# Performance work log

Measured on AMD Instinct MI355X. Metric: run time of the kernel, lower is better.

The kernel has to match this reference:

```python
import jax, jax.numpy as jnp
import numpy as np

VOCAB, VDIM, DDIM, BATCH = 50257, 300, 512, 16


def setup_inputs() -> dict:
    key = jax.random.key(0)
    k1, k2, k3, k4, k5 = jax.random.split(key, 5)
    return {
        "decoder_hidden": jax.random.normal(k1, (BATCH, DDIM), dtype=jnp.float32),
        "embedding_vocab": jax.random.normal(k2, (VOCAB, VDIM), dtype=jnp.float32),
        "W_dec": jax.random.normal(k3, (VDIM, DDIM), dtype=jnp.float32) * (1.0 / np.sqrt(DDIM)),
        "b_dec": jax.random.normal(k4, (VDIM,), dtype=jnp.float32) * 0.01,
        "W_full": jax.random.normal(k5, (VDIM,), dtype=jnp.float32) * (1.0 / np.sqrt(VDIM)),
        "b_full": jnp.zeros((), dtype=jnp.float32),
    }


def reference(decoder_hidden, embedding_vocab, W_dec, b_dec, W_full, b_full):
    # query: (B, vocab_dim) = decoder_att(decoder_hidden)
    query = decoder_hidden @ W_dec.T + b_dec
    # additive scores: relu(vocab + query) projected to scalar -> (B, V)
    hidden = jax.nn.relu(embedding_vocab[None, :, :] + query[:, None, :])  # (B, V, D)
    att = jnp.einsum("bvd,d->bv", hidden, W_full) + b_full
    alpha = jax.nn.softmax(att, axis=1)  # softmax over vocab
    # weighted sum of vocab embeddings: (B, vocab_dim)
    attention_weighted_encoding = jnp.einsum("bv,vd->bd", alpha, embedding_vocab)
    return attention_weighted_encoding, alpha
```

## Files before the change

kernel.cpp:

```cpp
#include <hip/hip_runtime.h>

constexpr int V  = 50257;
constexpr int D  = 300;
constexpr int KD = 512;
constexpr int B  = 16;

constexpr int ROWS = 64;
constexpr int NB_ATT = (V + ROWS - 1) / ROWS;
constexpr int NT = 5;
constexpr int NC  = 512;
constexpr int RPC = (V + NC - 1) / NC;

constexpr float NEG_HUGE = -1.0e30f;

constexpr size_t WS_QT   = 0;
constexpr size_t WS_STAT = 4800;
constexpr size_t WS_MS   = WS_STAT + (size_t)NB_ATT * 32;
constexpr size_t WS_PART = WS_MS + 32;
constexpr size_t WS_TMP  = WS_PART + (size_t)NC * 4800;

struct f4 { float v[4]; };
__device__ __forceinline__ f4 ld4(const float* p) {
    float4 t = *(const float4*)p;
    return {t.x, t.y, t.z, t.w};
}

#define AS1 __attribute__((address_space(1)))
#define AS3 __attribute__((address_space(3)))
#define DPPF(x, CTRL) __int_as_float(__builtin_amdgcn_mov_dpp(__float_as_int(x), (CTRL), 0xF, 0xF, false))

__global__ void __launch_bounds__(256) k_query(
    const float* __restrict__ dh, const float* __restrict__ Wdec,
    const float* __restrict__ bdec, float* __restrict__ q_t)
{
    int wid  = (blockIdx.x * 256 + threadIdx.x) >> 6;
    int lane = threadIdx.x & 63;
    if (wid >= D * B) return;
    int d = wid >> 4, b = wid & 15;
    const float* wrow = Wdec + (size_t)d * KD;
    const float* hrow = dh + (size_t)b * KD;
    float s = 0.f;
    for (int k = lane; k < KD; k += 64) s += wrow[k] * hrow[k];
    #pragma unroll
    for (int off = 32; off; off >>= 1) s += __shfl_down(s, off, 64);
    if (lane == 0) q_t[d * 16 + b] = s + bdec[d];
}

__global__ void __launch_bounds__(256) k_att(
    const float* __restrict__ E, const float* __restrict__ q_t,
    const float* __restrict__ wf, const float* __restrict__ bf,
    float* __restrict__ att, float* __restrict__ blkstats)
{
    __shared__ float se[3 * 4096];
    __shared__ float sq[5120];
    __shared__ float sw[320];

    const int t    = threadIdx.x;
    const int slot = t & 15;
    const int rg   = t >> 4;
    const int s4   = slot << 2;
    const int v0   = blockIdx.x * ROWS;

    for (int i = t; i < 5120; i += 256) {
        int d = i >> 4, b = i & 15;
        int bq = b >> 2, bl = b & 3;
        float v = (d < D) ? q_t[d * 16 + b] : 0.f;
        int P = (d >> 1) * 8 + ((((d & 1) << 2) | bq) ^ ((d >> 2) & 7));
        sq[P * 4 + bl] = v;
    }
    for (int i = t; i < 320; i += 256) sw[i] = (i < D) ? wf[i] : 0.f;

    int xq[2][4];
    #pragma unroll
    for (int i1 = 0; i1 < 2; ++i1)
        #pragma unroll
        for (int bq = 0; bq < 4; ++bq)
            xq[i1][bq] = slot * 64 + 4 * ((((i1 << 2) | bq)) ^ (slot & 7));

    float acc[4][16];
    #pragma unroll
    for (int j = 0; j < 4; ++j)
        #pragma unroll
        for (int b = 0; b < 16; ++b) acc[j][b] = 0.f;

    __syncthreads();

#define STAGE(TT, BI) do {                                                    \
    int dd = (TT) * 64 + s4;                                                  \
    if (dd >= D) dd = 0;                         \
    _Pragma("unroll")                                                         \
    for (int jj = 0; jj < 4; ++jj) {                                          \
        int row = v0 + jj * 16 + rg;                                          \
        if (row >= V) row = V - 1;                                            \
        const float* src = E + (size_t)row * D + dd;                          \
        float* lb = se + (BI) * 4096 + jj * 1024 + (t << 2);                  \
        __builtin_amdgcn_global_load_lds((const AS1 void*)src,                \
                                         (AS3 void*)lb, 16, 0, 0);            \
    }                                                                         \
} while (0)

#define COMPUTE(TT, BI) do {                                                  \
    const float* buf = se + (BI) * 4096;                                      \
    f4 ej[4];                                                                 \
    _Pragma("unroll")                                                         \
    for (int j = 0; j < 4; ++j) ej[j] = ld4(buf + rg * 64 + j * 1024 + s4);   \
    f4 wv = ld4(sw + (TT) * 64 + s4);                                         \
    const float* sqt = sq + (TT) * 1024;                                      \
    _Pragma("unroll")                                                         \
    for (int i = 0; i < 4; ++i) {                                             \
        float wi = wv.v[i];                                                   \
        _Pragma("unroll")                                                     \
        for (int bq = 0; bq < 4; ++bq) {                                      \
            f4 qv = ld4(sqt + (i >> 1) * 32 + xq[i & 1][bq]);                 \
            _Pragma("unroll")                                                 \
            for (int j = 0; j < 4; ++j) {                                     \
                float e = ej[j].v[i];                                         \
                _Pragma("unroll")                                             \
                for (int bl = 0; bl < 4; ++bl)                                \
                    acc[j][bq * 4 + bl] =                                     \
                        fmaf(fmaxf(e + qv.v[bl], 0.f), wi,                    \
                             acc[j][bq * 4 + bl]);                            \
            }                                                                 \
        }                                                                     \
    }                                                                         \
} while (0)

    STAGE(0, 0);
    STAGE(1, 1);
    for (int tt = 0; tt < NT; ++tt) {
        __builtin_amdgcn_sched_barrier(0);
        if (tt < NT - 1) asm volatile("s_waitcnt vmcnt(4)" ::: "memory");
        else             asm volatile("s_waitcnt vmcnt(0)" ::: "memory");
        __builtin_amdgcn_s_barrier();
        __builtin_amdgcn_sched_barrier(0);
        if (tt + 2 < NT) STAGE(tt + 2, (tt + 2) % 3);
        COMPUTE(tt, tt % 3);
    }
#undef STAGE
#undef COMPUTE

    #pragma unroll
    for (int j = 0; j < 4; ++j)
        #pragma unroll
        for (int b = 0; b < 16; ++b) {
            float x = acc[j][b];
            x += DPPF(x, 0xB1);
            x += DPPF(x, 0x4E);
            acc[j][b] = x;
        }
    const int c = slot & 3;
    float kept[4][4];
    #pragma unroll
    for (int j = 0; j < 4; ++j)
        #pragma unroll
        for (int kk = 0; kk < 4; ++kk) {
            float x = (c == 0) ? acc[j][kk]
                    : (c == 1) ? acc[j][4 + kk]
                    : (c == 2) ? acc[j][8 + kk]
                    :            acc[j][12 + kk];
            x += __shfl_xor(x, 4, 64);
            x += __shfl_xor(x, 8, 64);
            kept[j][kk] = x;
        }

    __syncthreads();
    float* smsM = se;
    float* smsS = se + 1024;

    const float bfull = bf[0];
    const int g = (t >> 6) * 16 + (rg & 3) * 4 + (slot >> 2);
    const int jown = slot >> 2;
    const int rowown = v0 + rg + 16 * jown;
    const bool okown = rowown < V;

    #pragma unroll
    for (int kk = 0; kk < 4; ++kk) {
        const int b = 4 * c + kk;
        float x = ((jown == 0) ? kept[0][kk] : (jown == 1) ? kept[1][kk]
                 : (jown == 2) ? kept[2][kk] : kept[3][kk]) + bfull;
        if (okown) att[(size_t)b * V + rowown] = x;
        smsM[g * 16 + b] = okown ? x : NEG_HUGE;
        smsS[g * 16 + b] = okown ? 1.f : 0.f;
    }
    __syncthreads();
    if (t < 64) {
        int b = t & 15, q4 = t >> 4;
        float m = NEG_HUGE, s = 0.f;
        for (int u = 0; u < 16; ++u) {
            int gg = q4 * 16 + u;
            float mg = smsM[gg * 16 + b], sg = smsS[gg * 16 + b];
            float mn = fmaxf(m, mg);
            s = s * __expf(m - mn) + sg * __expf(mg - mn);
            m = mn;
        }
        se[2048 + q4 * 16 + b] = m;
        se[2112 + q4 * 16 + b] = s;
    }
    __syncthreads();
    if (t < 16) {
        float m = NEG_HUGE, s = 0.f;
        #pragma unroll
        for (int q4 = 0; q4 < 4; ++q4) {
            float mg = se[2048 + q4 * 16 + t], sg = se[2112 + q4 * 16 + t];
            float mn = fmaxf(m, mg);
            s = s * __expf(m - mn) + sg * __expf(mg - mn);
            m = mn;
        }
        blkstats[((size_t)blockIdx.x * 16 + t) * 2]     = m;
        blkstats[((size_t)blockIdx.x * 16 + t) * 2 + 1] = s;
    }
}

__global__ void __launch_bounds__(64) k_combine(
    const float* __restrict__ blkstats, float* __restrict__ MS)
{
    int b = blockIdx.x, lane = threadIdx.x;
    float m = NEG_HUGE;
    for (int cc = lane; cc < NB_ATT; cc += 64)
        m = fmaxf(m, blkstats[(size_t)(cc * 16 + b) * 2]);
    #pragma unroll
    for (int off = 32; off; off >>= 1) m = fmaxf(m, __shfl_xor(m, off, 64));
    float s = 0.f;
    for (int cc = lane; cc < NB_ATT; cc += 64)
        s += blkstats[(size_t)(cc * 16 + b) * 2 + 1] *
             __expf(blkstats[(size_t)(cc * 16 + b) * 2] - m);
    #pragma unroll
    for (int off = 32; off; off >>= 1) s += __shfl_xor(s, off, 64);
    if (lane == 0) { MS[b * 2] = m; MS[b * 2 + 1] = 1.f / s; }
}

__global__ void __launch_bounds__(320) k_awsum(
    const float* __restrict__ E, float* __restrict__ att,
    const float* __restrict__ MS, float* __restrict__ partials)
{
    __shared__ float sal[RPC * 16];
    int c = blockIdx.x, t = threadIdx.x;
    int v0 = c * RPC;
    int n = V - v0;
    if (n > RPC) n = RPC;
    if (n < 0) n = 0;

    for (int i = t; i < RPC * 16; i += 320) {
        int b = i / RPC, vv = i - b * RPC;
        float a = 0.f;
        if (vv < n) {
            float M = MS[b * 2], invS = MS[b * 2 + 1];
            size_t gi = (size_t)b * V + v0 + vv;
            a = __expf(att[gi] - M) * invS;
            att[gi] = a;
        }
        sal[vv * 16 + b] = a;
    }
    __syncthreads();

    if (t < D) {
        float acc[16];
        #pragma unroll
        for (int b = 0; b < 16; ++b) acc[b] = 0.f;
        #pragma unroll 4
        for (int vv = 0; vv < n; ++vv) {
            float e = E[(size_t)(v0 + vv) * D + t];
            const float* ap = sal + vv * 16;
            f4 a0 = ld4(ap), a1 = ld4(ap + 4), a2 = ld4(ap + 8), a3 = ld4(ap + 12);
            #pragma unroll
            for (int b = 0; b < 4; ++b) {
                acc[b]      = fmaf(a0.v[b], e, acc[b]);
                acc[b + 4]  = fmaf(a1.v[b], e, acc[b + 4]);
                acc[b + 8]  = fmaf(a2.v[b], e, acc[b + 8]);
                acc[b + 12] = fmaf(a3.v[b], e, acc[b + 12]);
            }
        }
        #pragma unroll
        for (int b = 0; b < 16; ++b)
            partials[(size_t)c * 4800 + b * D + t] = acc[b];
    }
}

__global__ void __launch_bounds__(256) k_red1(
    const float* __restrict__ partials, float* __restrict__ tmp)
{
    int o4 = blockIdx.x * 256 + threadIdx.x;
    if (o4 >= 1200) return;
    int y = blockIdx.y;
    float4 s = {0.f, 0.f, 0.f, 0.f};
    for (int c = y * 32; c < y * 32 + 32; ++c) {
        float4 p = *(const float4*)(partials + (size_t)c * 4800 + o4 * 4);
        s.x += p.x; s.y += p.y; s.z += p.z; s.w += p.w;
    }
    *(float4*)(tmp + (size_t)y * 4800 + o4 * 4) = s;
}

__global__ void __launch_bounds__(256) k_red2(
    const float* __restrict__ tmp, float* __restrict__ out)
{
    int o4 = blockIdx.x * 256 + threadIdx.x;
    if (o4 >= 1200) return;
    float4 s = {0.f, 0.f, 0.f, 0.f};
    #pragma unroll
    for (int y = 0; y < 16; ++y) {
        float4 p = *(const float4*)(tmp + (size_t)y * 4800 + o4 * 4);
        s.x += p.x; s.y += p.y; s.z += p.z; s.w += p.w;
    }
    *(float4*)(out + o4 * 4) = s;
}

extern "C" void kernel_launch(void* const* d_in, const int* in_sizes, int n_in,
                              void* d_out, int out_size, void* d_ws, size_t ws_size,
                              hipStream_t stream) {
    const float* dh   = (const float*)d_in[0];
    const float* E    = (const float*)d_in[1];
    const float* Wdec = (const float*)d_in[2];
    const float* bdec = (const float*)d_in[3];
    const float* wf   = (const float*)d_in[4];
    const float* bf   = (const float*)d_in[5];
    float* out = (float*)d_out;
    float* ws  = (float*)d_ws;

    float* q_t   = ws + WS_QT;
    float* stats = ws + WS_STAT;
    float* MS    = ws + WS_MS;
    float* part  = ws + WS_PART;
    float* tmp   = ws + WS_TMP;
    float* att   = out + 4800;

    k_query<<<(D * B + 3) / 4, 256, 0, stream>>>(dh, Wdec, bdec, q_t);
    k_att<<<NB_ATT, 256, 0, stream>>>(E, q_t, wf, bf, att, stats);
    k_combine<<<B, 64, 0, stream>>>(stats, MS);
    k_awsum<<<NC, 320, 0, stream>>>(E, att, MS, part);
    k_red1<<<dim3(5, 16), 256, 0, stream>>>(part, tmp);
    k_red2<<<5, 256, 0, stream>>>(tmp, out);
}
```

Before: 91.56 us.

## Restructure attention-score kernel with register-resident query, packed FMA and online softmax

The score kernel now keeps the query and W_full slices in registers as float2 vectors and uses packed max/FMA operations. It stages contiguous 16-row chunks of the embedding into double-buffered LDS instead of column-tiled triple buffers. Row sums are reduced with cross-lane shuffles, and running softmax max/sum statistics are kept per thread, which replaces the earlier two-level LDS reduction. The weighted-sum kernel switches to 448 chunks with more unrolling, with the reduction split adjusted to match. This trades the prior register-tiled outer-product reuse for fewer LDS reads of the query, at the cost of extra shuffles and more block syncs per chunk.

Result: faster. 87.66 us (-4.3%).

```diff
diff --git a/kernel.cpp b/kernel.cpp
--- a/kernel.cpp
+++ b/kernel.cpp
@@ -6,18 +6,19 @@
 constexpr int B  = 16;
 
 constexpr int ROWS = 64;
-constexpr int NB_ATT = (V + ROWS - 1) / ROWS;
-constexpr int NT = 5;
-constexpr int NC  = 512;
-constexpr int RPC = (V + NC - 1) / NC;
+constexpr int NBLK = (V + ROWS - 1) / ROWS;
+constexpr int NC  = 448;
+constexpr int RPC = 113;
 
 constexpr float NEG_HUGE = -1.0e30f;
 
 constexpr size_t WS_QT   = 0;
-constexpr size_t WS_STAT = 4800;
-constexpr size_t WS_MS   = WS_STAT + (size_t)NB_ATT * 32;
+constexpr size_t WS_STAT = 5120;
+constexpr size_t WS_MS   = WS_STAT + (size_t)NBLK * 32;
 constexpr size_t WS_PART = WS_MS + 32;
 constexpr size_t WS_TMP  = WS_PART + (size_t)NC * 4800;
+
+typedef float v2f __attribute__((ext_vector_type(2)));
 
 struct f4 { float v[4]; };
 __device__ __forceinline__ f4 ld4(const float* p) {
@@ -27,7 +28,6 @@
 
 #define AS1 __attribute__((address_space(1)))
 #define AS3 __attribute__((address_space(3)))
-#define DPPF(x, CTRL) __int_as_float(__builtin_amdgcn_mov_dpp(__float_as_int(x), (CTRL), 0xF, 0xF, false))
 
 __global__ void __launch_bounds__(256) k_query(
     const float* __restrict__ dh, const float* __restrict__ Wdec,
@@ -35,177 +35,154 @@
 {
     int wid  = (blockIdx.x * 256 + threadIdx.x) >> 6;
     int lane = threadIdx.x & 63;
-    if (wid >= D * B) return;
+    if (wid >= 320 * 16) return;
     int d = wid >> 4, b = wid & 15;
-    const float* wrow = Wdec + (size_t)d * KD;
-    const float* hrow = dh + (size_t)b * KD;
     float s = 0.f;
-    for (int k = lane; k < KD; k += 64) s += wrow[k] * hrow[k];
-    #pragma unroll
-    for (int off = 32; off; off >>= 1) s += __shfl_down(s, off, 64);
-    if (lane == 0) q_t[d * 16 + b] = s + bdec[d];
-}
-
-__global__ void __launch_bounds__(256) k_att(
+    if (d < D) {
+        const float* wrow = Wdec + (size_t)d * KD;
+        const float* hrow = dh + (size_t)b * KD;
+        for (int k = lane; k < KD; k += 64) s += wrow[k] * hrow[k];
+        #pragma unroll
+        for (int off = 32; off; off >>= 1) s += __shfl_down(s, off, 64);
+        s += bdec[d];
+    }
+    if (lane == 0) q_t[d * 16 + b] = (d < D) ? s : 0.f;
+}
+
+__global__ void __launch_bounds__(256, 2) k_att(
     const float* __restrict__ E, const float* __restrict__ q_t,
     const float* __restrict__ wf, const float* __restrict__ bf,
     float* __restrict__ att, float* __restrict__ blkstats)
 {
-    __shared__ float se[3 * 4096];
-    __shared__ float sq[5120];
-    __shared__ float sw[320];
+    __shared__ __align__(16) float seE[2][4832];
+    __shared__ float satt[256];
+    __shared__ float sms[128];
 
     const int t    = threadIdx.x;
     const int slot = t & 15;
-    const int rg   = t >> 4;
-    const int s4   = slot << 2;
+    const int bg   = (t >> 4) & 3;
+    const int wv   = t >> 6;
     const int v0   = blockIdx.x * ROWS;
 
-    for (int i = t; i < 5120; i += 256) {
-        int d = i >> 4, b = i & 15;
-        int bq = b >> 2, bl = b & 3;
-        float v = (d < D) ? q_t[d * 16 + b] : 0.f;
-        int P = (d >> 1) * 8 + ((((d & 1) << 2) | bq) ^ ((d >> 2) & 7));
-        sq[P * 4 + bl] = v;
-    }
-    for (int i = t; i < 320; i += 256) sw[i] = (i < D) ? wf[i] : 0.f;
-
-    int xq[2][4];
-    #pragma unroll
-    for (int i1 = 0; i1 < 2; ++i1)
-        #pragma unroll
-        for (int bq = 0; bq < 4; ++bq)
-            xq[i1][bq] = slot * 64 + 4 * ((((i1 << 2) | bq)) ^ (slot & 7));
-
-    float acc[4][16];
-    #pragma unroll
-    for (int j = 0; j < 4; ++j)
-        #pragma unroll
-        for (int b = 0; b < 16; ++b) acc[j][b] = 0.f;
-
-    __syncthreads();
-
-#define STAGE(TT, BI) do {                                                    \
-    int dd = (TT) * 64 + s4;                                                  \
-    if (dd >= D) dd = 0;                         \
+    if (t < 32) { seE[0][4800 + t] = 0.f; seE[1][4800 + t] = 0.f; }
+
+    v2f q2[40];
+    #pragma unroll
+    for (int k = 0; k < 5; ++k)
+        #pragma unroll
+        for (int i = 0; i < 4; ++i) {
+            int d = k * 64 + slot * 4 + i;
+            f4 qv = ld4(q_t + d * 16 + bg * 4);
+            q2[(k * 4 + i) * 2]     = (v2f){qv.v[0], qv.v[1]};
+            q2[(k * 4 + i) * 2 + 1] = (v2f){qv.v[2], qv.v[3]};
+        }
+    f4 wreg[5];
+    #pragma unroll
+    for (int k = 0; k < 4; ++k) wreg[k] = ld4(wf + k * 64 + slot * 4);
+    if (slot < 11) wreg[4] = ld4(wf + 256 + slot * 4);
+    else { wreg[4].v[0] = wreg[4].v[1] = wreg[4].v[2] = wreg[4].v[3] = 0.f; }
+    const float bfull = bf[0];
+
+    float m_r[4], s_r[4];
+    #pragma unroll
+    for (int j = 0; j < 4; ++j) { m_r[j] = NEG_HUGE; s_r[j] = 0.f; }
+
+#define STAGE(S) do {                                                         \
+    int nr = V - (v0 + (S) * 16); if (nr > 16) nr = 16;                       \
+    int nflt = nr * 300;                                                      \
+    const float* src = E + (size_t)(v0 + (S) * 16) * 300;                     \
+    float* dst = &seE[(S) & 1][0];                                            \
     _Pragma("unroll")                                                         \
-    for (int jj = 0; jj < 4; ++jj) {                                          \
-        int row = v0 + jj * 16 + rg;                                          \
-        if (row >= V) row = V - 1;                                            \
-        const float* src = E + (size_t)row * D + dd;                          \
-        float* lb = se + (BI) * 4096 + jj * 1024 + (t << 2);                  \
-        __builtin_amdgcn_global_load_lds((const AS1 void*)src,                \
-                                         (AS3 void*)lb, 16, 0, 0);            \
+    for (int kk = 0; kk < 5; ++kk) {                                          \
+        int o = kk * 1024 + t * 4;                                            \
+        if (o < nflt)                                                         \
+            __builtin_amdgcn_global_load_lds((const AS1 void*)(src + o),      \
+                                             (AS3 void*)(dst + o), 16, 0, 0); \
     }                                                                         \
 } while (0)
 
-#define COMPUTE(TT, BI) do {                                                  \
-    const float* buf = se + (BI) * 4096;                                      \
-    f4 ej[4];                                                                 \
-    _Pragma("unroll")                                                         \
-    for (int j = 0; j < 4; ++j) ej[j] = ld4(buf + rg * 64 + j * 1024 + s4);   \
-    f4 wv = ld4(sw + (TT) * 64 + s4);                                         \
-    const float* sqt = sq + (TT) * 1024;                                      \
+#define MACK(EV, K) do {                                                      \
     _Pragma("unroll")                                                         \
     for (int i = 0; i < 4; ++i) {                                             \
-        float wi = wv.v[i];                                                   \
-        _Pragma("unroll")                                                     \
-        for (int bq = 0; bq < 4; ++bq) {                                      \
-            f4 qv = ld4(sqt + (i >> 1) * 32 + xq[i & 1][bq]);                 \
-            _Pragma("unroll")                                                 \
-            for (int j = 0; j < 4; ++j) {                                     \
-                float e = ej[j].v[i];                                         \
-                _Pragma("unroll")                                             \
-                for (int bl = 0; bl < 4; ++bl)                                \
-                    acc[j][bq * 4 + bl] =                                     \
-                        fmaf(fmaxf(e + qv.v[bl], 0.f), wi,                    \
-                             acc[j][bq * 4 + bl]);                            \
-            }                                                                 \
-        }                                                                     \
+        v2f eb  = {EV.v[i], EV.v[i]};                                         \
+        v2f wv2 = {wreg[K].v[i], wreg[K].v[i]};                               \
+        a0 = __builtin_elementwise_fma(                                       \
+            __builtin_elementwise_max(eb + q2[(K * 4 + i) * 2], z2), wv2, a0);\
+        a1 = __builtin_elementwise_fma(                                       \
+            __builtin_elementwise_max(eb + q2[(K * 4 + i) * 2 + 1], z2), wv2, a1);\
     }                                                                         \
 } while (0)
 
-    STAGE(0, 0);
-    STAGE(1, 1);
-    for (int tt = 0; tt < NT; ++tt) {
-        __builtin_amdgcn_sched_barrier(0);
-        if (tt < NT - 1) asm volatile("s_waitcnt vmcnt(4)" ::: "memory");
-        else             asm volatile("s_waitcnt vmcnt(0)" ::: "memory");
-        __builtin_amdgcn_s_barrier();
-        __builtin_amdgcn_sched_barrier(0);
-        if (tt + 2 < NT) STAGE(tt + 2, (tt + 2) % 3);
-        COMPUTE(tt, tt % 3);
+#define ONLINE(J, X) do {                                                     \
+    float mn = fmaxf(m_r[J], (X));                                            \
+    s_r[J] = s_r[J] * __expf(m_r[J] - mn) + (ok ? __expf((X) - mn) : 0.f);    \
+    m_r[J] = mn;                                                              \
+} while (0)
+
+#define COMPUTE(S) do {                                                       \
+    const float* bufc = &seE[(S) & 1][0];                                     \
+    _Pragma("unroll")                                                         \
+    for (int rr = 0; rr < 4; ++rr) {                                          \
+        const int lr = wv + 4 * rr;                                           \
+        const float* er = bufc + lr * 300 + slot * 4;                         \
+        f4 e0 = ld4(er);       f4 e1 = ld4(er + 64);  f4 e2 = ld4(er + 128);  \
+        f4 e3 = ld4(er + 192); f4 e4 = ld4(er + 256);                         \
+        v2f a0 = {0.f, 0.f}, a1 = {0.f, 0.f};                                 \
+        v2f z2 = {0.f, 0.f};                                                  \
+        MACK(e0, 0); MACK(e1, 1); MACK(e2, 2); MACK(e3, 3); MACK(e4, 4);      \
+        float x0 = a0[0], x1 = a0[1], x2 = a1[0], x3 = a1[1];                 \
+        _Pragma("unroll")                                                     \
+        for (int sh = 1; sh <= 8; sh <<= 1) {                                 \
+            x0 += __shfl_xor(x0, sh, 64); x1 += __shfl_xor(x1, sh, 64);       \
+            x2 += __shfl_xor(x2, sh, 64); x3 += __shfl_xor(x3, sh, 64);       \
+        }                                                                     \
+        const int vr = v0 + (S) * 16 + lr;                                    \
+        const bool ok = vr < V;                                               \
+        x0 = ok ? x0 + bfull : NEG_HUGE;                                      \
+        x1 = ok ? x1 + bfull : NEG_HUGE;                                      \
+        x2 = ok ? x2 + bfull : NEG_HUGE;                                      \
+        x3 = ok ? x3 + bfull : NEG_HUGE;                                      \
+        ONLINE(0, x0); ONLINE(1, x1); ONLINE(2, x2); ONLINE(3, x3);           \
+        if (slot == lr)                                                       \
+            *(float4*)(satt + lr * 16 + bg * 4) = make_float4(x0, x1, x2, x3);\
+    }                                                                         \
+} while (0)
+
+    STAGE(0);
+    __syncthreads();
+
+    #pragma unroll
+    for (int S = 0; S < 4; ++S) {
+        if (S < 3) STAGE(S + 1);
+        COMPUTE(S);
+        __syncthreads();
+        {
+            int b = t >> 4, r = t & 15;
+            int vr2 = v0 + S * 16 + r;
+            float val = satt[r * 16 + b];
+            if (vr2 < V) att[(size_t)b * V + vr2] = val;
+        }
+        __syncthreads();
     }
 #undef STAGE
+#undef MACK
+#undef ONLINE
 #undef COMPUTE
 
-    #pragma unroll
-    for (int j = 0; j < 4; ++j)
-        #pragma unroll
-        for (int b = 0; b < 16; ++b) {
-            float x = acc[j][b];
-            x += DPPF(x, 0xB1);
-            x += DPPF(x, 0x4E);
-            acc[j][b] = x;
-        }
-    const int c = slot & 3;
-    float kept[4][4];
-    #pragma unroll
-    for (int j = 0; j < 4; ++j)
-        #pragma unroll
-        for (int kk = 0; kk < 4; ++kk) {
-            float x = (c == 0) ? acc[j][kk]
-                    : (c == 1) ? acc[j][4 + kk]
-                    : (c == 2) ? acc[j][8 + kk]
-                    :            acc[j][12 + kk];
-            x += __shfl_xor(x, 4, 64);
-            x += __shfl_xor(x, 8, 64);
-            kept[j][kk] = x;
-        }
-
+    if (slot == 0) {
+        *(float4*)(sms + wv * 16 + bg * 4)      = make_float4(m_r[0], m_r[1], m_r[2], m_r[3]);
+        *(float4*)(sms + 64 + wv * 16 + bg * 4) = make_float4(s_r[0], s_r[1], s_r[2], s_r[3]);
+    }
     __syncthreads();
-    float* smsM = se;
-    float* smsS = se + 1024;
-
-    const float bfull = bf[0];
-    const int g = (t >> 6) * 16 + (rg & 3) * 4 + (slot >> 2);
-    const int jown = slot >> 2;
-    const int rowown = v0 + rg + 16 * jown;
-    const bool okown = rowown < V;
-
-    #pragma unroll
-    for (int kk = 0; kk < 4; ++kk) {
-        const int b = 4 * c + kk;
-        float x = ((jown == 0) ? kept[0][kk] : (jown == 1) ? kept[1][kk]
-                 : (jown == 2) ? kept[2][kk] : kept[3][kk]) + bfull;
-        if (okown) att[(size_t)b * V + rowown] = x;
-        smsM[g * 16 + b] = okown ? x : NEG_HUGE;
-        smsS[g * 16 + b] = okown ? 1.f : 0.f;
-    }
-    __syncthreads();
-    if (t < 64) {
-        int b = t & 15, q4 = t >> 4;
+    if (t < 16) {
         float m = NEG_HUGE, s = 0.f;
-        for (int u = 0; u < 16; ++u) {
-            int gg = q4 * 16 + u;
-            float mg = smsM[gg * 16 + b], sg = smsS[gg * 16 + b];
+        #pragma unroll
+        for (int w = 0; w < 4; ++w) {
+            float mg = sms[w * 16 + t], sg = sms[64 + w * 16 + t];
             float mn = fmaxf(m, mg);
             s = s * __expf(m - mn) + sg * __expf(mg - mn);
             m = mn;
         }
-        se[2048 + q4 * 16 + b] = m;
-        se[2112 + q4 * 16 + b] = s;
-    }
-    __syncthreads();
-    if (t < 16) {
-        float m = NEG_HUGE, s = 0.f;
-        #pragma unroll
-        for (int q4 = 0; q4 < 4; ++q4) {
-            float mg = se[2048 + q4 * 16 + t], sg = se[2112 + q4 * 16 + t];
-            float mn = fmaxf(m, mg);
-            s = s * __expf(m - mn) + sg * __expf(mg - mn);
-            m = mn;
-        }
         blkstats[((size_t)blockIdx.x * 16 + t) * 2]     = m;
         blkstats[((size_t)blockIdx.x * 16 + t) * 2 + 1] = s;
     }
@@ -216,12 +193,12 @@
 {
     int b = blockIdx.x, lane = threadIdx.x;
     float m = NEG_HUGE;
-    for (int cc = lane; cc < NB_ATT; cc += 64)
+    for (int cc = lane; cc < NBLK; cc += 64)
         m = fmaxf(m, blkstats[(size_t)(cc * 16 + b) * 2]);
     #pragma unroll
     for (int off = 32; off; off >>= 1) m = fmaxf(m, __shfl_xor(m, off, 64));
     float s = 0.f;
-    for (int cc = lane; cc < NB_ATT; cc += 64)
+    for (int cc = lane; cc < NBLK; cc += 64)
         s += blkstats[(size_t)(cc * 16 + b) * 2 + 1] *
              __expf(blkstats[(size_t)(cc * 16 + b) * 2] - m);
     #pragma unroll
@@ -257,7 +234,7 @@
         float acc[16];
         #pragma unroll
         for (int b = 0; b < 16; ++b) acc[b] = 0.f;
-        #pragma unroll 4
+        #pragma unroll 8
         for (int vv = 0; vv < n; ++vv) {
             float e = E[(size_t)(v0 + vv) * D + t];
             const float* ap = sal + vv * 16;
@@ -283,7 +260,7 @@
     if (o4 >= 1200) return;
     int y = blockIdx.y;
     float4 s = {0.f, 0.f, 0.f, 0.f};
-    for (int c = y * 32; c < y * 32 + 32; ++c) {
+    for (int c = y * 28; c < y * 28 + 28; ++c) {
         float4 p = *(const float4*)(partials + (size_t)c * 4800 + o4 * 4);
         s.x += p.x; s.y += p.y; s.z += p.z; s.w += p.w;
     }
@@ -323,8 +300,8 @@
     float* tmp   = ws + WS_TMP;
     float* att   = out + 4800;
 
-    k_query<<<(D * B + 3) / 4, 256, 0, stream>>>(dh, Wdec, bdec, q_t);
-    k_att<<<NB_ATT, 256, 0, stream>>>(E, q_t, wf, bf, att, stats);
+    k_query<<<(320 * 16) / 4, 256, 0, stream>>>(dh, Wdec, bdec, q_t);
+    k_att<<<NBLK, 256, 0, stream>>>(E, q_t, wf, bf, att, stats);
     k_combine<<<B, 64, 0, stream>>>(stats, MS);
     k_awsum<<<NC, 320, 0, stream>>>(E, att, MS, part);
     k_red1<<<dim3(5, 16), 256, 0, stream>>>(part, tmp);
```
